# Performance work log

Measured on AMD Instinct MI355X. Metric: run time of the kernel, lower is better.

## Reference

```python
import jax, jax.numpy as jnp
import numpy as np

H = 128   # hidden_size
IN = 4    # input_size
OUT = 4   # linear output dim


def _lstm_layer(x, Wih, Whh, bih, bhh):
    """Single PyTorch-convention LSTM layer (gate order i,f,g,o), batch_first.
    x: [B,T,D] -> hidden states [B,T,H]."""
    B, T, _ = x.shape
    Hd = Whh.shape[1]
    # Precompute input contribution to gates for all timesteps: [B,T,4H]
    xg = jnp.einsum('btd,gd->btg', x, Wih) + bih + bhh
    xg = jnp.swapaxes(xg, 0, 1)  # [T,B,4H] for scan
    h0 = jnp.zeros((B, Hd), x.dtype)
    c0 = jnp.zeros((B, Hd), x.dtype)

    def step(carry, gx):
        h, c = carry
        g = gx + h @ Whh.T            # [B,4H]
        i, f, gg, o = jnp.split(g, 4, axis=-1)
        i = jax.nn.sigmoid(i)
        f = jax.nn.sigmoid(f)
        gg = jnp.tanh(gg)
        o = jax.nn.sigmoid(o)
        c = f * c + i * gg
        h = o * jnp.tanh(c)
        return (h, c), h

    _, hs = jax.lax.scan(step, (h0, c0), xg)  # hs: [T,B,H]
    return jnp.swapaxes(hs, 0, 1)             # [B,T,H]


def setup_inputs() -> dict:
    key = jax.random.key(0)
    ks = jax.random.split(key, 11)
    B, T = 256, 2048
    s = 1.0 / np.sqrt(H)  # torch LSTM/Linear default init scale
    u = lambda k, shape: jax.random.uniform(k, shape, jnp.float32, -s, s)
    return dict(
        x=jax.random.normal(ks[0], (B, T, IN), jnp.float32),
        Wih0=u(ks[1], (4 * H, IN)),  Whh0=u(ks[2], (4 * H, H)),
        bih0=u(ks[3], (4 * H,)),     bhh0=u(ks[4], (4 * H,)),
        Wih1=u(ks[5], (4 * H, H)),   Whh1=u(ks[6], (4 * H, H)),
        bih1=u(ks[7], (4 * H,)),     bhh1=u(ks[8], (4 * H,)),
        Wlin=u(ks[9], (OUT, H)),     blin=u(ks[10], (OUT,)),
    )


def reference(x, Wih0, Whh0, bih0, bhh0, Wih1, Whh1, bih1, bhh1, Wlin, blin):
    h1 = _lstm_layer(x, Wih0, Whh0, bih0, bhh0)    # layer 0
    zs = _lstm_layer(h1, Wih1, Whh1, bih1, bhh1)   # layer 1, [B,T,H]
    z = zs[:, -1]                                  # last hidden state [B,H]
    v = jnp.einsum('bth,oh->bto', zs, Wlin) + blin # [B,T,4]
    return (v, z)
```

## Files before the change

### kernel.cpp

```cpp
#include <hip/hip_runtime.h>

#define BB 256
#define TT 2048
#define HH 128
#define HP 136
#define G4 512
#define INW 4
#define OUTW 4
#define TC 56
#define NT 512

typedef _Float16 f16x8 __attribute__((ext_vector_type(8)));
typedef float    f32x4 __attribute__((ext_vector_type(4)));

#define MFMA(A,B,C) __builtin_amdgcn_mfma_f32_16x16x32_f16((A),(B),(C),0,0,0)

__device__ __forceinline__ float sigm(float x)  { return __fdividef(1.f, 1.f + __expf(-x)); }
__device__ __forceinline__ float tanh_(float x) { return __fdividef(2.f, 1.f + __expf(-2.f*x)) - 1.f; }


#define LDF(dst, wrj, kk) do {                                                 \
    const float* p_ = Mp_ + (size_t)(wrj) * HH + (kk)*32 + (kq << 3);          \
    const float4 lo_ = *(const float4*)p_;                                     \
    const float4 hi_ = *(const float4*)(p_ + 4);                               \
    dst = (f16x8){(_Float16)lo_.x,(_Float16)lo_.y,(_Float16)lo_.z,             \
                  (_Float16)lo_.w,(_Float16)hi_.x,(_Float16)hi_.y,             \
                  (_Float16)hi_.z,(_Float16)hi_.w}; } while (0)

#define LOADW(M) do { const float* Mp_ = (M);                                  \
    LDF(w00, wr0,      0); LDF(w01, wr0,      1); LDF(w02, wr0,      2); LDF(w03, wr0,      3); \
    LDF(w10, wr0 + 4,  0); LDF(w11, wr0 + 4,  1); LDF(w12, wr0 + 4,  2); LDF(w13, wr0 + 4,  3); \
    LDF(w20, wr0 + 8,  0); LDF(w21, wr0 + 8,  1); LDF(w22, wr0 + 8,  2); LDF(w23, wr0 + 8,  3); \
    LDF(w30, wr0 + 12, 0); LDF(w31, wr0 + 12, 1); LDF(w32, wr0 + 12, 2); LDF(w33, wr0 + 12, 3); \
} while (0)

#define RSTEP(HB) do {                                                         \
    f16x8 hv_;                                                                 \
    hv_ = *(const f16x8*)((HB) + (kq << 3));                                   \
    a0 = MFMA(w00, hv_, a0); a1 = MFMA(w10, hv_, a1);                          \
    a2 = MFMA(w20, hv_, a2); a3 = MFMA(w30, hv_, a3);                          \
    hv_ = *(const f16x8*)((HB) + 32 + (kq << 3));                              \
    a0 = MFMA(w01, hv_, a0); a1 = MFMA(w11, hv_, a1);                          \
    a2 = MFMA(w21, hv_, a2); a3 = MFMA(w31, hv_, a3);                          \
    hv_ = *(const f16x8*)((HB) + 64 + (kq << 3));                              \
    a0 = MFMA(w02, hv_, a0); a1 = MFMA(w12, hv_, a1);                          \
    a2 = MFMA(w22, hv_, a2); a3 = MFMA(w32, hv_, a3);                          \
    hv_ = *(const f16x8*)((HB) + 96 + (kq << 3));                              \
    a0 = MFMA(w03, hv_, a0); a1 = MFMA(w13, hv_, a1);                          \
    a2 = MFMA(w23, hv_, a2); a3 = MFMA(w33, hv_, a3); } while (0)

#define UPDSEL(CJ, HN) do {                                                    \
    f32x4 av_;                                                                 \
    _Pragma("unroll")                                                          \
    for (int e_ = 0; e_ < 4; ++e_) {                                           \
        const float t01_ = j1 ? a1[e_] : a0[e_];                               \
        const float t23_ = j1 ? a3[e_] : a2[e_];                               \
        av_[e_] = j2 ? t23_ : t01_;                                            \
    }                                                                          \
    const float i_ = sigm(av_[0]);                                             \
    const float f_ = sigm(av_[1]);                                             \
    const float g_ = tanh_(av_[2]);                                            \
    const float o_ = sigm(av_[3]);                                             \
    CJ = f_ * CJ + i_ * g_;                                                    \
    HN = o_ * tanh_(CJ); } while (0)

extern "C" __global__ void
__attribute__((amdgpu_flat_work_group_size(NT, NT)))
lstm2_fused(const float* __restrict__ x,
            const float* __restrict__ Wih0, const float* __restrict__ Whh0,
            const float* __restrict__ bih0, const float* __restrict__ bhh0,
            const float* __restrict__ Wih1, const float* __restrict__ Whh1,
            const float* __restrict__ bih1, const float* __restrict__ bhh1,
            const float* __restrict__ Wlin, const float* __restrict__ blin,
            float* __restrict__ out)
{
    __shared__ __align__(16) _Float16 h1h[(TC + 9) * HP];
    __shared__ __align__(16) float    buf[TC * G4];
    __shared__ __align__(16) _Float16 h2h[2 * HH];
    __shared__ float xc[TC * INW];
    __shared__ float b0c[G4], b1c[G4];
    __shared__ float wlc[OUTW * HH];
    __shared__ float blc[OUTW];

    const int i    = threadIdx.x;
    const int w    = i >> 6;
    const int lane = i & 63;
    const int r    = lane & 15;
    const int kq   = lane >> 4;
    const int b    = blockIdx.x;

    const int wr0 = ((r & 3) << 7) | (r >> 2) | (w << 4);

    const bool j1 = (r & 1), j2 = (r & 2);
    const int  myu = (w << 4) | ((r & 3) << 2) | kq;
    const bool own = (r < 4);

    if (i < G4) { b0c[i] = bih0[i] + bhh0[i]; b1c[i] = bih1[i] + bhh1[i]; }
    wlc[i] = Wlin[i];
    if (i < OUTW) blc[i] = blin[i];
    if (i < HH) { h1h[i] = (_Float16)0.f; h2h[i] = (_Float16)0.f; }

    float c1 = 0.f, c2 = 0.f;
    f16x8 w00, w01, w02, w03, w10, w11, w12, w13,
          w20, w21, w22, w23, w30, w31, w32, w33;

    const float* xb   = x   + (size_t)b * TT * INW;
    float*       vout = out + (size_t)b * TT * OUTW;
    float*       zout = out + (size_t)BB * TT * OUTW + (size_t)b * HH;

    for (int t0 = 0; t0 < TT; t0 += TC) {
        const int tc = (TT - t0 < TC) ? (TT - t0) : TC;

        if (t0 > 0 && i < HH) h1h[i] = h1h[TC * HP + i];
        for (int j = i; j < tc * INW; j += NT) xc[j] = xb[t0 * INW + j];
        __syncthreads();

        for (int idx = i; idx < tc * G4; idx += NT) {
            const int t = idx >> 9, rg = idx & 511;
            const int row = ((rg & 3) << 7) | (rg >> 2);
            const float4 wv = *(const float4*)(Wih0 + (size_t)row * INW);
            const float4 xv = *(const float4*)(xc + t * INW);
            buf[idx] = b0c[row] + wv.x*xv.x + wv.y*xv.y + wv.z*xv.z + wv.w*xv.w;
        }
        LOADW(Whh0);
        __syncthreads();

        for (int t = 0; t < tc; ++t) {
            const float* bp = buf + t * G4 + (w << 6) + (kq << 2);
            f32x4 a0 = *(const f32x4*)(bp);
            f32x4 a1 = *(const f32x4*)(bp + 16);
            f32x4 a2 = *(const f32x4*)(bp + 32);
            f32x4 a3 = *(const f32x4*)(bp + 48);
            RSTEP(h1h + t * HP);
            float hn;
            UPDSEL(c1, hn);
            if (own) h1h[(t + 1) * HP + myu] = (_Float16)hn;
            __syncthreads();
        }

        LOADW(Wih1);
        const int ntb = (tc + 15) >> 4;
        for (int tb = 0; tb < ntb; ++tb) {
            f32x4 a0 = {0.f,0.f,0.f,0.f}, a1 = {0.f,0.f,0.f,0.f},
                  a2 = {0.f,0.f,0.f,0.f}, a3 = {0.f,0.f,0.f,0.f};
            const _Float16* ha = h1h + (tb * 16 + r + 1) * HP;
            f16x8 tv;
            tv = *(const f16x8*)(ha + (kq << 3));
            a0 = MFMA(tv, w00, a0); a1 = MFMA(tv, w10, a1);
            a2 = MFMA(tv, w20, a2); a3 = MFMA(tv, w30, a3);
            tv = *(const f16x8*)(ha + 32 + (kq << 3));
            a0 = MFMA(tv, w01, a0); a1 = MFMA(tv, w11, a1);
            a2 = MFMA(tv, w21, a2); a3 = MFMA(tv, w31, a3);
            tv = *(const f16x8*)(ha + 64 + (kq << 3));
            a0 = MFMA(tv, w02, a0); a1 = MFMA(tv, w12, a1);
            a2 = MFMA(tv, w22, a2); a3 = MFMA(tv, w32, a3);
            tv = *(const f16x8*)(ha + 96 + (kq << 3));
            a0 = MFMA(tv, w03, a0); a1 = MFMA(tv, w13, a1);
            a2 = MFMA(tv, w23, a2); a3 = MFMA(tv, w33, a3);
            const float b_0 = b1c[wr0],     b_1 = b1c[wr0 + 4];
            const float b_2 = b1c[wr0 + 8], b_3 = b1c[wr0 + 12];
            #pragma unroll
            for (int e = 0; e < 4; ++e) {
                const int tl = tb * 16 + (kq << 2) + e;
                if (tl < tc) {
                    float* bq = buf + tl * G4 + (w << 6) + r;
                    bq[0]  = a0[e] + b_0;
                    bq[16] = a1[e] + b_1;
                    bq[32] = a2[e] + b_2;
                    bq[48] = a3[e] + b_3;
                }
            }
        }
        __syncthreads();

        LOADW(Whh1);
        for (int t = 0; t < tc; ++t) {
            const int rb = (t & 1) * HH, wbuf = rb ^ HH;
            const float* bp = buf + t * G4 + (w << 6) + (kq << 2);
            f32x4 a0 = *(const f32x4*)(bp);
            f32x4 a1 = *(const f32x4*)(bp + 16);
            f32x4 a2 = *(const f32x4*)(bp + 32);
            f32x4 a3 = *(const f32x4*)(bp + 48);
            RSTEP(h2h + rb);
            float hn;
            UPDSEL(c2, hn);
            if (own) {
                h2h[wbuf + myu] = (_Float16)hn;
                if (t0 + t == TT - 1) zout[myu] = hn;
            }
            __syncthreads();
            if (i < 256) {
                const int o = i >> 6, l = i & 63;
                float p2 = (float)h2h[wbuf + l]      * wlc[o*HH + l]
                         + (float)h2h[wbuf + 64 + l] * wlc[o*HH + 64 + l];
                p2 += __shfl_xor(p2, 32);
                p2 += __shfl_xor(p2, 16);
                p2 += __shfl_xor(p2, 8);
                p2 += __shfl_xor(p2, 4);
                p2 += __shfl_xor(p2, 2);
                p2 += __shfl_xor(p2, 1);
                if (l == 0) vout[(size_t)(t0 + t) * OUTW + o] = p2 + blc[o];
            }
        }
    }
}

extern "C" void kernel_launch(void* const* d_in, const int* in_sizes, int n_in,
                              void* d_out, int out_size, void* d_ws, size_t ws_size,
                              hipStream_t stream) {
    const float* x    = (const float*)d_in[0];
    const float* Wih0 = (const float*)d_in[1];
    const float* Whh0 = (const float*)d_in[2];
    const float* bih0 = (const float*)d_in[3];
    const float* bhh0 = (const float*)d_in[4];
    const float* Wih1 = (const float*)d_in[5];
    const float* Whh1 = (const float*)d_in[6];
    const float* bih1 = (const float*)d_in[7];
    const float* bhh1 = (const float*)d_in[8];
    const float* Wlin = (const float*)d_in[9];
    const float* blin = (const float*)d_in[10];
    float* out = (float*)d_out;

    lstm2_fused<<<dim3(BB), dim3(NT), 0, stream>>>(
        x, Wih0, Whh0, bih0, bhh0, Wih1, Whh1, bih1, bhh1, Wlin, blin, out);
}
```

Measured before the change: 3.048 ms.

## Defer output projection to per-chunk batch and keep biases in registers

Layer-1 hidden states are now kept for the whole time chunk in a shared ring buffer. The per-timestep Linear projection with its shuffle reduction moves out of the serial recurrence into one parallel pass after each chunk. The input projection for layer 0 now reads x straight from global memory, with each thread's Wih0 row and the biases held in registers, so the xc staging, the bias shared arrays and one barrier are gone. This shortens the latency-bound recurrent loop, at the cost of more shared memory and a redundant global x read per thread.

```diff
diff --git a/kernel.cpp b/kernel.cpp
--- a/kernel.cpp
+++ b/kernel.cpp
@@ -76,11 +76,8 @@
 {
     __shared__ __align__(16) _Float16 h1h[(TC + 9) * HP];
     __shared__ __align__(16) float    buf[TC * G4];
-    __shared__ __align__(16) _Float16 h2h[2 * HH];
-    __shared__ float xc[TC * INW];
-    __shared__ float b0c[G4], b1c[G4];
-    __shared__ float wlc[OUTW * HH];
-    __shared__ float blc[OUTW];
+    __shared__ __align__(16) _Float16 h2r[(TC + 1) * HH];
+    __shared__ __align__(16) float    wlc[OUTW * HH];
 
     const int i    = threadIdx.x;
     const int w    = i >> 6;
@@ -90,15 +87,23 @@
     const int b    = blockIdx.x;
 
     const int wr0 = ((r & 3) << 7) | (r >> 2) | (w << 4);
-
     const bool j1 = (r & 1), j2 = (r & 2);
     const int  myu = (w << 4) | ((r & 3) << 2) | kq;
     const bool own = (r < 4);
 
-    if (i < G4) { b0c[i] = bih0[i] + bhh0[i]; b1c[i] = bih1[i] + bhh1[i]; }
+    const int  rg_row = ((i & 3) << 7) | (i >> 2);
+    const float4 wv   = *(const float4*)(Wih0 + (size_t)rg_row * INW);
+    const float  b0r  = bih0[rg_row] + bhh0[rg_row];
+    const float  bb0  = bih1[wr0]      + bhh1[wr0];
+    const float  bb1  = bih1[wr0 + 4]  + bhh1[wr0 + 4];
+    const float  bb2  = bih1[wr0 + 8]  + bhh1[wr0 + 8];
+    const float  bb3  = bih1[wr0 + 12] + bhh1[wr0 + 12];
+    const int   po   = (i >> 2) & 3;
+    const int   part = i & 3;
+    const float bl   = blin[po];
+
     wlc[i] = Wlin[i];
-    if (i < OUTW) blc[i] = blin[i];
-    if (i < HH) { h1h[i] = (_Float16)0.f; h2h[i] = (_Float16)0.f; }
+    if (i < HH) { h1h[i] = (_Float16)0.f; h2r[i] = (_Float16)0.f; }
 
     float c1 = 0.f, c2 = 0.f;
     f16x8 w00, w01, w02, w03, w10, w11, w12, w13,
@@ -111,16 +116,13 @@
     for (int t0 = 0; t0 < TT; t0 += TC) {
         const int tc = (TT - t0 < TC) ? (TT - t0) : TC;
 
-        if (t0 > 0 && i < HH) h1h[i] = h1h[TC * HP + i];
-        for (int j = i; j < tc * INW; j += NT) xc[j] = xb[t0 * INW + j];
-        __syncthreads();
-
-        for (int idx = i; idx < tc * G4; idx += NT) {
-            const int t = idx >> 9, rg = idx & 511;
-            const int row = ((rg & 3) << 7) | (rg >> 2);
-            const float4 wv = *(const float4*)(Wih0 + (size_t)row * INW);
-            const float4 xv = *(const float4*)(xc + t * INW);
-            buf[idx] = b0c[row] + wv.x*xv.x + wv.y*xv.y + wv.z*xv.z + wv.w*xv.w;
+        if (t0 > 0 && i < HH) {
+            h1h[i] = h1h[TC * HP + i];
+            h2r[i] = h2r[TC * HH + i];
+        }
+        for (int t = 0; t < tc; ++t) {
+            const float4 xv = *(const float4*)(xb + (size_t)(t0 + t) * INW);
+            buf[t * G4 + i] = b0r + wv.x*xv.x + wv.y*xv.y + wv.z*xv.z + wv.w*xv.w;
         }
         LOADW(Whh0);
         __syncthreads();
@@ -157,17 +159,15 @@
             tv = *(const f16x8*)(ha + 96 + (kq << 3));
             a0 = MFMA(tv, w03, a0); a1 = MFMA(tv, w13, a1);
             a2 = MFMA(tv, w23, a2); a3 = MFMA(tv, w33, a3);
-            const float b_0 = b1c[wr0],     b_1 = b1c[wr0 + 4];
-            const float b_2 = b1c[wr0 + 8], b_3 = b1c[wr0 + 12];
             #pragma unroll
             for (int e = 0; e < 4; ++e) {
                 const int tl = tb * 16 + (kq << 2) + e;
                 if (tl < tc) {
                     float* bq = buf + tl * G4 + (w << 6) + r;
-                    bq[0]  = a0[e] + b_0;
-                    bq[16] = a1[e] + b_1;
-                    bq[32] = a2[e] + b_2;
-                    bq[48] = a3[e] + b_3;
+                    bq[0]  = a0[e] + bb0;
+                    bq[16] = a1[e] + bb1;
+                    bq[32] = a2[e] + bb2;
+                    bq[48] = a3[e] + bb3;
                 }
             }
         }
@@ -175,32 +175,37 @@
 
         LOADW(Whh1);
         for (int t = 0; t < tc; ++t) {
-            const int rb = (t & 1) * HH, wbuf = rb ^ HH;
             const float* bp = buf + t * G4 + (w << 6) + (kq << 2);
             f32x4 a0 = *(const f32x4*)(bp);
             f32x4 a1 = *(const f32x4*)(bp + 16);
             f32x4 a2 = *(const f32x4*)(bp + 32);
             f32x4 a3 = *(const f32x4*)(bp + 48);
-            RSTEP(h2h + rb);
+            RSTEP(h2r + t * HH);
             float hn;
             UPDSEL(c2, hn);
             if (own) {
-                h2h[wbuf + myu] = (_Float16)hn;
+                h2r[(t + 1) * HH + myu] = (_Float16)hn;
                 if (t0 + t == TT - 1) zout[myu] = hn;
             }
             __syncthreads();
-            if (i < 256) {
-                const int o = i >> 6, l = i & 63;
-                float p2 = (float)h2h[wbuf + l]      * wlc[o*HH + l]
-                         + (float)h2h[wbuf + 64 + l] * wlc[o*HH + 64 + l];
-                p2 += __shfl_xor(p2, 32);
-                p2 += __shfl_xor(p2, 16);
-                p2 += __shfl_xor(p2, 8);
-                p2 += __shfl_xor(p2, 4);
-                p2 += __shfl_xor(p2, 2);
-                p2 += __shfl_xor(p2, 1);
-                if (l == 0) vout[(size_t)(t0 + t) * OUTW + o] = p2 + blc[o];
+        }
+
+        for (int t = i >> 4; t < tc; t += NT >> 4) {
+            const f16x8*  hp = (const f16x8*)(h2r + (t + 1) * HH + part * 32);
+            const float4* wp = (const float4*)(wlc + po * HH + part * 32);
+            float s = 0.f;
+            #pragma unroll
+            for (int q = 0; q < 4; ++q) {
+                const f16x8 hv = hp[q];
+                const float4 wa = wp[2*q], wb2 = wp[2*q + 1];
+                s += (float)hv[0]*wa.x  + (float)hv[1]*wa.y
+                   + (float)hv[2]*wa.z  + (float)hv[3]*wa.w
+                   + (float)hv[4]*wb2.x + (float)hv[5]*wb2.y
+                   + (float)hv[6]*wb2.z + (float)hv[7]*wb2.w;
             }
+            s += __shfl_xor(s, 1);
+            s += __shfl_xor(s, 2);
+            if (part == 0) vout[(size_t)(t0 + t) * OUTW + po] = s + bl;
         }
     }
 }
```

Measured after the change: 3.191 ms. +4.7%, slower.
